# Kernel tuning notes

Hardware: AMD Instinct MI355X
Metric: run time of the kernel (lower is better)

Reference implementation:

```python
import jax, jax.numpy as jnp
import numpy as np

B, N, C, A, H, W = 2, 5, 64, 2, 128, 256
COMM_THRESH = 0.01  # args['communication']['threshold']
SEL_TOPK = 2        # args['selector']['topk']


def _grid_sample(src, theta, Ho, Wo, mode):
    """torch affine_grid + grid_sample (align_corners=True, zero padding).
    src: (L,C,Hs,Ws), theta: (L,2,3) normalized affine, out: (L,C,Ho,Wo)."""
    L, Cc, Hs, Ws = src.shape
    xs = jnp.linspace(-1.0, 1.0, Wo, dtype=src.dtype)
    ys = jnp.linspace(-1.0, 1.0, Ho, dtype=src.dtype)
    gx, gy = jnp.meshgrid(xs, ys)                      # (Ho,Wo)
    base = jnp.stack([gx, gy, jnp.ones_like(gx)], -1)  # (Ho,Wo,3)
    coords = jnp.einsum('lij,hwj->lhwi', theta, base)  # (L,Ho,Wo,2)
    ix = (coords[..., 0] + 1.0) * 0.5 * (Ws - 1)
    iy = (coords[..., 1] + 1.0) * 0.5 * (Hs - 1)
    flat = src.reshape(L, Cc, Hs * Ws)

    def gather(yi, xi):
        valid = ((yi >= 0) & (yi < Hs) & (xi >= 0) & (xi < Ws)).astype(src.dtype)
        idx = jnp.clip(yi, 0, Hs - 1) * Ws + jnp.clip(xi, 0, Ws - 1)
        idx = jnp.broadcast_to(idx.reshape(L, 1, Ho * Wo), (L, Cc, Ho * Wo))
        v = jnp.take_along_axis(flat, idx, axis=2).reshape(L, Cc, Ho, Wo)
        return v * valid[:, None]

    if mode == 'nearest':
        return gather(jnp.round(iy).astype(jnp.int32), jnp.round(ix).astype(jnp.int32))
    x0 = jnp.floor(ix)
    y0 = jnp.floor(iy)
    wx = (ix - x0)[:, None]  # (L,1,Ho,Wo)
    wy = (iy - y0)[:, None]
    x0i = x0.astype(jnp.int32); y0i = y0.astype(jnp.int32)
    v00 = gather(y0i, x0i)
    v01 = gather(y0i, x0i + 1)
    v10 = gather(y0i + 1, x0i)
    v11 = gather(y0i + 1, x0i + 1)
    return (v00 * (1 - wy) * (1 - wx) + v01 * (1 - wy) * wx
            + v10 * wy * (1 - wx) + v11 * wy * wx)


def setup_inputs() -> dict:
    key = jax.random.key(0)
    k1, k2, k3 = jax.random.split(key, 3)
    x = jax.random.normal(k1, (B * N, C, H, W), jnp.float32)
    psm = jax.random.normal(k2, (B * N, A, H, W), jnp.float32)
    # near-identity affines: identity rotation + small random translation; diag = exact identity
    t = jax.random.uniform(k3, (B, N, N, 2), jnp.float32, -0.3, 0.3)
    t = t.at[:, jnp.arange(N), jnp.arange(N)].set(0.0)
    eye = jnp.tile(jnp.array([[1., 0., 0.], [0., 1., 0.]], jnp.float32), (B, N, N, 1, 1))
    nam = eye.at[..., 2].set(t)  # (B,N,N,2,3)
    return {"x": x, "psm_single": psm, "normalized_affine_matrix": nam, "record_len": N}


def reference(x, psm_single, normalized_affine_matrix, record_len):
    n = record_len
    sumN, c, h, w = x.shape
    b = normalized_affine_matrix.shape[0]
    # T_ego: row 0 of each batch's pairwise transform block, one (2,3) per agent
    theta = normalized_affine_matrix[:, 0].reshape(b * n, 2, 3).astype(x.dtype)
    vis = _grid_sample(jnp.ones((sumN, 1, h, w), x.dtype), theta, h, w, 'nearest')
    conf_w = _grid_sample(psm_single.astype(x.dtype), theta, h, w, 'bilinear')
    feats_w = _grid_sample(x, theta, h, w, 'bilinear')
    # communication masks: sigmoid confidence, max over anchors, threshold; ego always 1
    comm_map = jax.nn.sigmoid(conf_w).max(axis=1, keepdims=True)  # (sumN,1,h,w)
    comm = (comm_map > COMM_THRESH).astype(x.dtype)
    comm = comm.reshape(b, n, 1, h, w).at[:, 0].set(1.0).reshape(sumN, 1, h, w)
    # selector: top-k nearest non-ego agents by translation distance (hard, eval mode)
    t = normalized_affine_matrix[:, 0, :, :2, 2]                  # (b,n,2)
    dist2 = jnp.sum(t * t, axis=-1).at[:, 0].set(jnp.inf)        # exclude ego
    _, idx = jax.lax.top_k(-dist2, SEL_TOPK)                      # (b,k)
    owner = jnp.zeros((b, n), x.dtype).at[jnp.arange(b)[:, None], idx].set(1.0)
    owner = owner.at[:, 0].set(1.0)                               # max with ego mask
    final = comm * owner.reshape(sumN, 1, 1, 1)
    wx = feats_w * final
    num = (final * vis).reshape(sumN, -1).sum(-1)
    den = jnp.maximum(vis.reshape(sumN, -1).sum(-1), 1.0)
    effective_rate = (num / den).mean()
    x_out = wx.reshape(b, n, c, h, w).max(axis=1)                 # MaxFusion over agents
    return x_out, effective_rate
```

## Files before the change

kernel.cpp:

```cpp
#include <hip/hip_runtime.h>
#include <math.h>

namespace {
constexpr int Bc = 2, Nc = 5, Cc = 64, Ac = 2, Hc = 128, Wc = 256;
constexpr int SUMN = Bc * Nc;
constexpr int HW = Hc * Wc;
constexpr float LOGIT_THRESH = -4.59511985013459f;
constexpr int CPT = 8;
constexpr int MASK_BLOCKS = (Bc * HW) / 256;

constexpr int OWNER_OFF = 64, PART_OFF = 128;
constexpr int MASK_BYTE_OFF = 11264;

__global__ void k_setup(const float* __restrict__ nam, float* __restrict__ wsf,
                        int* __restrict__ wsi) {
  int tid = threadIdx.x;
  if (tid < SUMN) {
    int b = tid / Nc, j = tid % Nc;
    const float* src = nam + (size_t)(b * Nc * Nc + j) * 6;
#pragma unroll
    for (int k = 0; k < 6; ++k) wsf[tid * 6 + k] = src[k];
    wsi[OWNER_OFF + tid] = (j == 0) ? 1 : 0;
  }
  __syncthreads();
  if (tid < Bc) {
    int b = tid;
    float d2[Nc];
    for (int j = 0; j < Nc; ++j) {
      float tx = nam[(size_t)(b * Nc * Nc + j) * 6 + 2];
      float ty = nam[(size_t)(b * Nc * Nc + j) * 6 + 5];
      d2[j] = tx * tx + ty * ty;
    }
    d2[0] = INFINITY;
    int i1 = -1; float b1 = INFINITY;
    for (int j = 0; j < Nc; ++j) if (d2[j] < b1) { b1 = d2[j]; i1 = j; }
    int i2 = -1; float b2 = INFINITY;
    for (int j = 0; j < Nc; ++j) if (j != i1 && d2[j] < b2) { b2 = d2[j]; i2 = j; }
    if (i1 >= 0) wsi[OWNER_OFF + b * Nc + i1] = 1;
    if (i2 >= 0) wsi[OWNER_OFF + b * Nc + i2] = 1;
  }
}

__global__ void __launch_bounds__(256) k_mask(const float* __restrict__ psm,
                                              const float* __restrict__ wsf,
                                              const int* __restrict__ wsi,
                                              int* __restrict__ partial,
                                              unsigned char* __restrict__ mask) {
  __shared__ int cnt[Nc * 2];
  int tid = threadIdx.x;
  if (tid < Nc * 2) cnt[tid] = 0;
  __syncthreads();

  int t = blockIdx.x * blockDim.x + tid;
  int b = t >> 15;
  int h = (t >> 8) & (Hc - 1);
  int w = t & (Wc - 1);
  float gx = -1.0f + (float)w * (2.0f / (Wc - 1));
  float gy = -1.0f + (float)h * (2.0f / (Hc - 1));
  unsigned m = 0;
#pragma unroll
  for (int j = 0; j < Nc; ++j) {
    int l = b * Nc + j;
    float t00 = wsf[l * 6 + 0], t01 = wsf[l * 6 + 1], t02 = wsf[l * 6 + 2];
    float t10 = wsf[l * 6 + 3], t11 = wsf[l * 6 + 4], t12 = wsf[l * 6 + 5];
    float cx = t00 * gx + t01 * gy + t02;
    float cy = t10 * gx + t11 * gy + t12;
    float ix = (cx + 1.0f) * 0.5f * (float)(Wc - 1);
    float iy = (cy + 1.0f) * 0.5f * (float)(Hc - 1);
    int rx = (int)rintf(ix), ry = (int)rintf(iy);
    int vis = (rx >= 0 && rx < Wc && ry >= 0 && ry < Hc) ? 1 : 0;
    int comm = 1;
    if (j != 0) {
      float x0f = floorf(ix), y0f = floorf(iy);
      float fx = ix - x0f, fy = iy - y0f;
      int x0 = (int)x0f, y0 = (int)y0f;
      int x1 = x0 + 1, y1 = y0 + 1;
      bool vx0 = (x0 >= 0) && (x0 < Wc), vx1 = (x1 >= 0) && (x1 < Wc);
      bool vy0 = (y0 >= 0) && (y0 < Hc), vy1 = (y1 >= 0) && (y1 < Hc);
      int cx0 = min(max(x0, 0), Wc - 1), cx1 = min(max(x1, 0), Wc - 1);
      int cy0 = min(max(y0, 0), Hc - 1), cy1 = min(max(y1, 0), Hc - 1);
      int o00 = cy0 * Wc + cx0, o01 = cy0 * Wc + cx1;
      int o10 = cy1 * Wc + cx0, o11 = cy1 * Wc + cx1;
      float w00 = (vy0 && vx0) ? (1.0f - fy) * (1.0f - fx) : 0.0f;
      float w01 = (vy0 && vx1) ? (1.0f - fy) * fx : 0.0f;
      float w10 = (vy1 && vx0) ? fy * (1.0f - fx) : 0.0f;
      float w11 = (vy1 && vx1) ? fy * fx : 0.0f;
      float vmax = -INFINITY;
#pragma unroll
      for (int a = 0; a < Ac; ++a) {
        const float* p = psm + (size_t)(l * Ac + a) * HW;
        float v = p[o00] * w00 + p[o01] * w01 + p[o10] * w10 + p[o11] * w11;
        vmax = fmaxf(vmax, v);
      }
      comm = (vmax > LOGIT_THRESH) ? 1 : 0;
    }
    int owner = wsi[OWNER_OFF + l];
    int fin = comm & owner;
    m |= (unsigned)fin << j;
    unsigned long long bv = __ballot(vis != 0);
    unsigned long long bf = __ballot((fin & vis) != 0);
    if ((tid & 63) == 0) {
      atomicAdd(&cnt[j * 2 + 0], (int)__popcll(bv));
      atomicAdd(&cnt[j * 2 + 1], (int)__popcll(bf));
    }
  }
  mask[t] = (unsigned char)m;
  __syncthreads();
  if (tid < Nc * 2) partial[blockIdx.x * (Nc * 2) + tid] = cnt[tid];
}

__global__ void __launch_bounds__(256) k_feat(const float* __restrict__ x,
                                              const float* __restrict__ wsf,
                                              const unsigned char* __restrict__ mask,
                                              float* __restrict__ out) {
  int t = blockIdx.x * blockDim.x + threadIdx.x;
  int w = t & (Wc - 1);
  int h = (t >> 8) & (Hc - 1);
  int c8 = (t >> 15) & (Cc / CPT - 1);
  int b = t >> 18;
  int pix = (b << 15) | (h << 8) | w;
  unsigned m = mask[pix];
  float gx = -1.0f + (float)w * (2.0f / (Wc - 1));
  float gy = -1.0f + (float)h * (2.0f / (Hc - 1));
  float best[CPT];
#pragma unroll
  for (int k = 0; k < CPT; ++k) best[k] = 0.0f;
#pragma unroll
  for (int j = 0; j < Nc; ++j) {
    if (m & (1u << j)) {
      int l = b * Nc + j;
      float t00 = wsf[l * 6 + 0], t01 = wsf[l * 6 + 1], t02 = wsf[l * 6 + 2];
      float t10 = wsf[l * 6 + 3], t11 = wsf[l * 6 + 4], t12 = wsf[l * 6 + 5];
      float cx = t00 * gx + t01 * gy + t02;
      float cy = t10 * gx + t11 * gy + t12;
      float ix = (cx + 1.0f) * 0.5f * (float)(Wc - 1);
      float iy = (cy + 1.0f) * 0.5f * (float)(Hc - 1);
      float x0f = floorf(ix), y0f = floorf(iy);
      float fx = ix - x0f, fy = iy - y0f;
      int x0 = (int)x0f, y0 = (int)y0f;
      int x1 = x0 + 1, y1 = y0 + 1;
      bool vx0 = (x0 >= 0) && (x0 < Wc), vx1 = (x1 >= 0) && (x1 < Wc);
      bool vy0 = (y0 >= 0) && (y0 < Hc), vy1 = (y1 >= 0) && (y1 < Hc);
      int cx0 = min(max(x0, 0), Wc - 1), cx1 = min(max(x1, 0), Wc - 1);
      int cy0 = min(max(y0, 0), Hc - 1), cy1 = min(max(y1, 0), Hc - 1);
      int o00 = cy0 * Wc + cx0, o01 = cy0 * Wc + cx1;
      int o10 = cy1 * Wc + cx0, o11 = cy1 * Wc + cx1;
      float w00 = (vy0 && vx0) ? (1.0f - fy) * (1.0f - fx) : 0.0f;
      float w01 = (vy0 && vx1) ? (1.0f - fy) * fx : 0.0f;
      float w10 = (vy1 && vx0) ? fy * (1.0f - fx) : 0.0f;
      float w11 = (vy1 && vx1) ? fy * fx : 0.0f;
      const float* p = x + ((size_t)(l * Cc + c8 * CPT)) * HW;
#pragma unroll
      for (int k = 0; k < CPT; ++k) {
        float val = p[o00] * w00 + p[o01] * w01 + p[o10] * w10 + p[o11] * w11;
        best[k] = fmaxf(best[k], val);
        p += HW;
      }
    }
  }
  size_t obase = ((size_t)(b * Cc + c8 * CPT)) * HW + (h << 8) + w;
#pragma unroll
  for (int k = 0; k < CPT; ++k) {
    __builtin_nontemporal_store(best[k], &out[obase + (size_t)k * HW]);
  }
}

__global__ void k_rate(const int* __restrict__ partial, float* __restrict__ out) {
  int lane = threadIdx.x;
  float s = 0.0f;
  for (int l = 0; l < SUMN; ++l) {
    int b = l / Nc, j = l % Nc;
    int vis = 0, num = 0;
#pragma unroll
    for (int k = 0; k < MASK_BLOCKS / Bc / 64; ++k) {
      int blk = b * (MASK_BLOCKS / Bc) + lane + 64 * k;
      vis += partial[blk * (Nc * 2) + j * 2 + 0];
      num += partial[blk * (Nc * 2) + j * 2 + 1];
    }
#pragma unroll
    for (int off = 32; off; off >>= 1) {
      vis += __shfl_down(vis, off);
      num += __shfl_down(num, off);
    }
    if (lane == 0) s += (float)num / fmaxf((float)vis, 1.0f);
  }
  if (lane == 0) out[(size_t)Bc * Cc * HW] = s / (float)SUMN;
}

}

extern "C" void kernel_launch(void* const* d_in, const int* in_sizes, int n_in,
                              void* d_out, int out_size, void* d_ws, size_t ws_size,
                              hipStream_t stream) {
  const float* x = (const float*)d_in[0];
  const float* psm = (const float*)d_in[1];
  const float* nam = (const float*)d_in[2];
  float* out = (float*)d_out;
  float* wsf = (float*)d_ws;
  int* wsi = (int*)d_ws;
  int* partial = wsi + PART_OFF;
  unsigned char* mask = (unsigned char*)d_ws + MASK_BYTE_OFF;

  hipLaunchKernelGGL(k_setup, dim3(1), dim3(64), 0, stream, nam, wsf, wsi);
  hipLaunchKernelGGL(k_mask, dim3(MASK_BLOCKS), dim3(256), 0, stream, psm, wsf, wsi, partial,
                     mask);
  hipLaunchKernelGGL(k_feat, dim3((Bc * (Cc / CPT) * HW) / 256), dim3(256), 0, stream, x, wsf,
                     mask, out);
  hipLaunchKernelGGL(k_rate, dim3(1), dim3(1), 0, stream, partial, out);
}
```

Before: 138.7 us.

## Fold setup and rate kernels into mask/feat, vectorize feat over 4 pixels

Removes the setup kernel by computing owner bits inline in the mask kernel and reading affines directly from the input. The rate reduction moves into an extra block of the feature kernel, cutting the launch count from four to two. The feature kernel now handles 4 adjacent pixels × 4 channels per thread, with a fast path that uses vector row loads when the 4 sample points are contiguous, plus 16-byte nontemporal stores. This adds register pressure and a divergent fallback path for non-contiguous samples.

```diff
diff --git a/kernel.cpp b/kernel.cpp
--- a/kernel.cpp
+++ b/kernel.cpp
@@ -6,44 +6,39 @@
 constexpr int SUMN = Bc * Nc;
 constexpr int HW = Hc * Wc;
 constexpr float LOGIT_THRESH = -4.59511985013459f;
-constexpr int CPT = 8;
 constexpr int MASK_BLOCKS = (Bc * HW) / 256;
-
-constexpr int OWNER_OFF = 64, PART_OFF = 128;
-constexpr int MASK_BYTE_OFF = 11264;
-
-__global__ void k_setup(const float* __restrict__ nam, float* __restrict__ wsf,
-                        int* __restrict__ wsi) {
-  int tid = threadIdx.x;
-  if (tid < SUMN) {
-    int b = tid / Nc, j = tid % Nc;
-    const float* src = nam + (size_t)(b * Nc * Nc + j) * 6;
-#pragma unroll
-    for (int k = 0; k < 6; ++k) wsf[tid * 6 + k] = src[k];
-    wsi[OWNER_OFF + tid] = (j == 0) ? 1 : 0;
-  }
-  __syncthreads();
-  if (tid < Bc) {
-    int b = tid;
-    float d2[Nc];
-    for (int j = 0; j < Nc; ++j) {
-      float tx = nam[(size_t)(b * Nc * Nc + j) * 6 + 2];
-      float ty = nam[(size_t)(b * Nc * Nc + j) * 6 + 5];
-      d2[j] = tx * tx + ty * ty;
-    }
-    d2[0] = INFINITY;
-    int i1 = -1; float b1 = INFINITY;
-    for (int j = 0; j < Nc; ++j) if (d2[j] < b1) { b1 = d2[j]; i1 = j; }
-    int i2 = -1; float b2 = INFINITY;
-    for (int j = 0; j < Nc; ++j) if (j != i1 && d2[j] < b2) { b2 = d2[j]; i2 = j; }
-    if (i1 >= 0) wsi[OWNER_OFF + b * Nc + i1] = 1;
-    if (i2 >= 0) wsi[OWNER_OFF + b * Nc + i2] = 1;
-  }
+constexpr int FEAT_BLOCKS = (Bc * (Cc / 4) * Hc * (Wc / 4)) / 256;
+
+constexpr int MASK_BYTE_OFF = 10240;
+
+typedef float f4v __attribute__((ext_vector_type(4)));
+
+__device__ __forceinline__ f4v load4u(const float* p) {
+  f4v r;
+  __builtin_memcpy(&r, p, sizeof(r));
+  return r;
+}
+
+__device__ __forceinline__ unsigned owner_bits(const float* __restrict__ nam, int b) {
+  float d2[Nc];
+#pragma unroll
+  for (int j = 0; j < Nc; ++j) {
+    float tx = nam[(size_t)(b * Nc * Nc + j) * 6 + 2];
+    float ty = nam[(size_t)(b * Nc * Nc + j) * 6 + 5];
+    d2[j] = tx * tx + ty * ty;
+  }
+  d2[0] = INFINITY;
+  int i1 = 1; float b1 = INFINITY;
+#pragma unroll
+  for (int j = 0; j < Nc; ++j) if (d2[j] < b1) { b1 = d2[j]; i1 = j; }
+  int i2 = 1; float b2 = INFINITY;
+#pragma unroll
+  for (int j = 0; j < Nc; ++j) if (j != i1 && d2[j] < b2) { b2 = d2[j]; i2 = j; }
+  return 1u | (1u << i1) | (1u << i2);
 }
 
 __global__ void __launch_bounds__(256) k_mask(const float* __restrict__ psm,
-                                              const float* __restrict__ wsf,
-                                              const int* __restrict__ wsi,
+                                              const float* __restrict__ nam,
                                               int* __restrict__ partial,
                                               unsigned char* __restrict__ mask) {
   __shared__ int cnt[Nc * 2];
@@ -51,20 +46,20 @@
   if (tid < Nc * 2) cnt[tid] = 0;
   __syncthreads();
 
-  int t = blockIdx.x * blockDim.x + tid;
-  int b = t >> 15;
+  int t = blockIdx.x * 256 + tid;
+  int b = __builtin_amdgcn_readfirstlane(t >> 15);
   int h = (t >> 8) & (Hc - 1);
   int w = t & (Wc - 1);
+  unsigned own = owner_bits(nam, b);
   float gx = -1.0f + (float)w * (2.0f / (Wc - 1));
   float gy = -1.0f + (float)h * (2.0f / (Hc - 1));
   unsigned m = 0;
 #pragma unroll
   for (int j = 0; j < Nc; ++j) {
     int l = b * Nc + j;
-    float t00 = wsf[l * 6 + 0], t01 = wsf[l * 6 + 1], t02 = wsf[l * 6 + 2];
-    float t10 = wsf[l * 6 + 3], t11 = wsf[l * 6 + 4], t12 = wsf[l * 6 + 5];
-    float cx = t00 * gx + t01 * gy + t02;
-    float cy = t10 * gx + t11 * gy + t12;
+    const float* th = nam + (size_t)(b * Nc * Nc + j) * 6;
+    float cx = th[0] * gx + th[1] * gy + th[2];
+    float cy = th[3] * gx + th[4] * gy + th[5];
     float ix = (cx + 1.0f) * 0.5f * (float)(Wc - 1);
     float iy = (cy + 1.0f) * 0.5f * (float)(Hc - 1);
     int rx = (int)rintf(ix), ry = (int)rintf(iy);
@@ -94,8 +89,7 @@
       }
       comm = (vmax > LOGIT_THRESH) ? 1 : 0;
     }
-    int owner = wsi[OWNER_OFF + l];
-    int fin = comm & owner;
+    int fin = comm & (int)((own >> j) & 1u);
     m |= (unsigned)fin << j;
     unsigned long long bv = __ballot(vis != 0);
     unsigned long long bf = __ballot((fin & vis) != 0);
@@ -110,81 +104,137 @@
 }
 
 __global__ void __launch_bounds__(256) k_feat(const float* __restrict__ x,
-                                              const float* __restrict__ wsf,
+                                              const float* __restrict__ nam,
                                               const unsigned char* __restrict__ mask,
+                                              const int* __restrict__ partial,
                                               float* __restrict__ out) {
-  int t = blockIdx.x * blockDim.x + threadIdx.x;
-  int w = t & (Wc - 1);
-  int h = (t >> 8) & (Hc - 1);
-  int c8 = (t >> 15) & (Cc / CPT - 1);
-  int b = t >> 18;
-  int pix = (b << 15) | (h << 8) | w;
-  unsigned m = mask[pix];
-  float gx = -1.0f + (float)w * (2.0f / (Wc - 1));
+  if (blockIdx.x == FEAT_BLOCKS) {
+    int lane = threadIdx.x;
+    if (lane < 64) {
+      float s = 0.0f;
+      for (int l = 0; l < SUMN; ++l) {
+        int b = l / Nc, j = l % Nc;
+        int vis = 0, num = 0;
+#pragma unroll
+        for (int k = 0; k < 2; ++k) {
+          int blk = b * (MASK_BLOCKS / Bc) + lane + 64 * k;
+          vis += partial[blk * (Nc * 2) + j * 2 + 0];
+          num += partial[blk * (Nc * 2) + j * 2 + 1];
+        }
+#pragma unroll
+        for (int off = 32; off; off >>= 1) {
+          vis += __shfl_down(vis, off);
+          num += __shfl_down(num, off);
+        }
+        if (lane == 0) s += (float)num / fmaxf((float)vis, 1.0f);
+      }
+      if (lane == 0) out[(size_t)Bc * Cc * HW] = s / (float)SUMN;
+    }
+    return;
+  }
+
+  int q = blockIdx.x * 256 + threadIdx.x;
+  int w0 = (q & 63) << 2;
+  int h = (q >> 6) & (Hc - 1);
+  int c4 = (q >> 13) & (Cc / 4 - 1);
+  int b = q >> 17;
+  int bs = __builtin_amdgcn_readfirstlane(b);
+
+  unsigned mm4;
+  __builtin_memcpy(&mm4, mask + (size_t)bs * HW + h * Wc + w0, 4);
+
   float gy = -1.0f + (float)h * (2.0f / (Hc - 1));
-  float best[CPT];
-#pragma unroll
-  for (int k = 0; k < CPT; ++k) best[k] = 0.0f;
+  float best[4][4];
+#pragma unroll
+  for (int c = 0; c < 4; ++c)
+#pragma unroll
+    for (int k = 0; k < 4; ++k) best[c][k] = 0.0f;
+
 #pragma unroll
   for (int j = 0; j < Nc; ++j) {
-    if (m & (1u << j)) {
-      int l = b * Nc + j;
-      float t00 = wsf[l * 6 + 0], t01 = wsf[l * 6 + 1], t02 = wsf[l * 6 + 2];
-      float t10 = wsf[l * 6 + 3], t11 = wsf[l * 6 + 4], t12 = wsf[l * 6 + 5];
+    if ((mm4 & (0x01010101u << j)) == 0) continue;
+    int l = bs * Nc + j;
+    const float* th = nam + (size_t)(bs * Nc * Nc + j) * 6;
+    float t00 = th[0], t01 = th[1], t02 = th[2];
+    float t10 = th[3], t11 = th[4], t12 = th[5];
+
+    float ix[4], iy[4], fx[4], fy[4];
+    int x0i[4], y0i[4];
+#pragma unroll
+    for (int k = 0; k < 4; ++k) {
+      float gx = -1.0f + (float)(w0 + k) * (2.0f / (Wc - 1));
       float cx = t00 * gx + t01 * gy + t02;
       float cy = t10 * gx + t11 * gy + t12;
-      float ix = (cx + 1.0f) * 0.5f * (float)(Wc - 1);
-      float iy = (cy + 1.0f) * 0.5f * (float)(Hc - 1);
-      float x0f = floorf(ix), y0f = floorf(iy);
-      float fx = ix - x0f, fy = iy - y0f;
-      int x0 = (int)x0f, y0 = (int)y0f;
-      int x1 = x0 + 1, y1 = y0 + 1;
-      bool vx0 = (x0 >= 0) && (x0 < Wc), vx1 = (x1 >= 0) && (x1 < Wc);
-      bool vy0 = (y0 >= 0) && (y0 < Hc), vy1 = (y1 >= 0) && (y1 < Hc);
-      int cx0 = min(max(x0, 0), Wc - 1), cx1 = min(max(x1, 0), Wc - 1);
-      int cy0 = min(max(y0, 0), Hc - 1), cy1 = min(max(y1, 0), Hc - 1);
-      int o00 = cy0 * Wc + cx0, o01 = cy0 * Wc + cx1;
-      int o10 = cy1 * Wc + cx0, o11 = cy1 * Wc + cx1;
-      float w00 = (vy0 && vx0) ? (1.0f - fy) * (1.0f - fx) : 0.0f;
-      float w01 = (vy0 && vx1) ? (1.0f - fy) * fx : 0.0f;
-      float w10 = (vy1 && vx0) ? fy * (1.0f - fx) : 0.0f;
-      float w11 = (vy1 && vx1) ? fy * fx : 0.0f;
-      const float* p = x + ((size_t)(l * Cc + c8 * CPT)) * HW;
-#pragma unroll
-      for (int k = 0; k < CPT; ++k) {
-        float val = p[o00] * w00 + p[o01] * w01 + p[o10] * w10 + p[o11] * w11;
-        best[k] = fmaxf(best[k], val);
+      ix[k] = (cx + 1.0f) * 0.5f * (float)(Wc - 1);
+      iy[k] = (cy + 1.0f) * 0.5f * (float)(Hc - 1);
+      float x0f = floorf(ix[k]), y0f = floorf(iy[k]);
+      fx[k] = ix[k] - x0f; fy[k] = iy[k] - y0f;
+      x0i[k] = (int)x0f; y0i[k] = (int)y0f;
+    }
+    int X0 = x0i[0], Y0 = y0i[0];
+    bool fast = (x0i[1] == X0 + 1) && (x0i[2] == X0 + 2) && (x0i[3] == X0 + 3) &&
+                (y0i[1] == Y0) && (y0i[2] == Y0) && (y0i[3] == Y0) &&
+                (X0 >= 0) && (X0 + 4 < Wc);
+    const float* xb = x + (size_t)(l * Cc + c4 * 4) * HW;
+
+    if (fast) {
+      bool vy0 = (Y0 >= 0) && (Y0 < Hc), vy1 = (Y0 + 1 >= 0) && (Y0 + 1 < Hc);
+      int cy0 = min(max(Y0, 0), Hc - 1), cy1 = min(max(Y0 + 1, 0), Hc - 1);
+      int r0off = cy0 * Wc + X0, r1off = cy1 * Wc + X0;
+      float wy0[4], wy1[4];
+#pragma unroll
+      for (int k = 0; k < 4; ++k) {
+        wy0[k] = vy0 ? (1.0f - fy[k]) : 0.0f;
+        wy1[k] = vy1 ? fy[k] : 0.0f;
+      }
+      const float* p = xb;
+#pragma unroll
+      for (int c = 0; c < 4; ++c) {
+        f4v a0 = load4u(p + r0off); float a0e = p[r0off + 4];
+        f4v a1 = load4u(p + r1off); float a1e = p[r1off + 4];
+        float r0[5] = {a0.x, a0.y, a0.z, a0.w, a0e};
+        float r1[5] = {a1.x, a1.y, a1.z, a1.w, a1e};
+#pragma unroll
+        for (int k = 0; k < 4; ++k) {
+          float val = wy0[k] * (r0[k] * (1.0f - fx[k]) + r0[k + 1] * fx[k]) +
+                      wy1[k] * (r1[k] * (1.0f - fx[k]) + r1[k + 1] * fx[k]);
+          val = ((mm4 >> (8 * k + j)) & 1u) ? val : 0.0f;
+          best[c][k] = fmaxf(best[c][k], val);
+        }
         p += HW;
       }
-    }
-  }
-  size_t obase = ((size_t)(b * Cc + c8 * CPT)) * HW + (h << 8) + w;
-#pragma unroll
-  for (int k = 0; k < CPT; ++k) {
-    __builtin_nontemporal_store(best[k], &out[obase + (size_t)k * HW]);
-  }
-}
-
-__global__ void k_rate(const int* __restrict__ partial, float* __restrict__ out) {
-  int lane = threadIdx.x;
-  float s = 0.0f;
-  for (int l = 0; l < SUMN; ++l) {
-    int b = l / Nc, j = l % Nc;
-    int vis = 0, num = 0;
-#pragma unroll
-    for (int k = 0; k < MASK_BLOCKS / Bc / 64; ++k) {
-      int blk = b * (MASK_BLOCKS / Bc) + lane + 64 * k;
-      vis += partial[blk * (Nc * 2) + j * 2 + 0];
-      num += partial[blk * (Nc * 2) + j * 2 + 1];
-    }
-#pragma unroll
-    for (int off = 32; off; off >>= 1) {
-      vis += __shfl_down(vis, off);
-      num += __shfl_down(num, off);
-    }
-    if (lane == 0) s += (float)num / fmaxf((float)vis, 1.0f);
-  }
-  if (lane == 0) out[(size_t)Bc * Cc * HW] = s / (float)SUMN;
+    } else {
+#pragma unroll
+      for (int k = 0; k < 4; ++k) {
+        if (((mm4 >> (8 * k + j)) & 1u) == 0) continue;
+        int x0 = x0i[k], y0 = y0i[k], x1 = x0 + 1, y1 = y0 + 1;
+        bool vx0 = (x0 >= 0) && (x0 < Wc), vx1 = (x1 >= 0) && (x1 < Wc);
+        bool vy0 = (y0 >= 0) && (y0 < Hc), vy1 = (y1 >= 0) && (y1 < Hc);
+        int cx0 = min(max(x0, 0), Wc - 1), cx1 = min(max(x1, 0), Wc - 1);
+        int cy0 = min(max(y0, 0), Hc - 1), cy1 = min(max(y1, 0), Hc - 1);
+        int o00 = cy0 * Wc + cx0, o01 = cy0 * Wc + cx1;
+        int o10 = cy1 * Wc + cx0, o11 = cy1 * Wc + cx1;
+        float w00 = (vy0 && vx0) ? (1.0f - fy[k]) * (1.0f - fx[k]) : 0.0f;
+        float w01 = (vy0 && vx1) ? (1.0f - fy[k]) * fx[k] : 0.0f;
+        float w10 = (vy1 && vx0) ? fy[k] * (1.0f - fx[k]) : 0.0f;
+        float w11 = (vy1 && vx1) ? fy[k] * fx[k] : 0.0f;
+        const float* p = xb;
+#pragma unroll
+        for (int c = 0; c < 4; ++c) {
+          float val = p[o00] * w00 + p[o01] * w01 + p[o10] * w10 + p[o11] * w11;
+          best[c][k] = fmaxf(best[c][k], val);
+          p += HW;
+        }
+      }
+    }
+  }
+
+  size_t obase = (size_t)(bs * Cc + c4 * 4) * HW + h * Wc + w0;
+#pragma unroll
+  for (int c = 0; c < 4; ++c) {
+    f4v v = {best[c][0], best[c][1], best[c][2], best[c][3]};
+    __builtin_nontemporal_store(v, (f4v*)(out + obase + (size_t)c * HW));
+  }
 }
 
 }
@@ -196,15 +246,10 @@
   const float* psm = (const float*)d_in[1];
   const float* nam = (const float*)d_in[2];
   float* out = (float*)d_out;
-  float* wsf = (float*)d_ws;
-  int* wsi = (int*)d_ws;
-  int* partial = wsi + PART_OFF;
+  int* partial = (int*)d_ws;
   unsigned char* mask = (unsigned char*)d_ws + MASK_BYTE_OFF;
 
-  hipLaunchKernelGGL(k_setup, dim3(1), dim3(64), 0, stream, nam, wsf, wsi);
-  hipLaunchKernelGGL(k_mask, dim3(MASK_BLOCKS), dim3(256), 0, stream, psm, wsf, wsi, partial,
-                     mask);
-  hipLaunchKernelGGL(k_feat, dim3((Bc * (Cc / CPT) * HW) / 256), dim3(256), 0, stream, x, wsf,
-                     mask, out);
-  hipLaunchKernelGGL(k_rate, dim3(1), dim3(1), 0, stream, partial, out);
-}
+  hipLaunchKernelGGL(k_mask, dim3(MASK_BLOCKS), dim3(256), 0, stream, psm, nam, partial, mask);
+  hipLaunchKernelGGL(k_feat, dim3(FEAT_BLOCKS + 1), dim3(256), 0, stream, x, nam, mask, partial,
+                     out);
+}
```

Result: no change. 139.6 us (+0.6%).
